# Kernel tuning notes

Hardware: AMD Instinct MI355X
Metric: run time of the kernel (lower is better)

## Reference

```python
import jax, jax.numpy as jnp
import numpy as np

B, DIN, E, FACTOR, STEPS, NH = 2048, 1024, 1024, 16, 3, 8
DH = E // NH
EPS = 1e-5


def layernorm(x, g, b):
    m = x.mean(-1, keepdims=True)
    v = ((x - m) ** 2).mean(-1, keepdims=True)
    return (x - m) / jnp.sqrt(v + EPS) * g + b


def setup_inputs() -> dict:
    key = jax.random.key(0)
    ks = iter(jax.random.split(key, 32))
    r = lambda shape, s=0.02: jax.random.normal(next(ks), shape, dtype=jnp.float32) * s
    F = E * FACTOR
    return {
        "image_feat": jax.random.normal(next(ks), (B, DIN), dtype=jnp.float32),
        "text_feat": jax.random.normal(next(ks), (B, DIN), dtype=jnp.float32),
        # fusion block
        "fc1_w": r((F, DIN)), "fc1_b": jnp.zeros((F,), jnp.float32),
        "fc2_w": r((F, DIN)), "fc2_b": jnp.zeros((F,), jnp.float32),
        "fc3_w": r((E, F)), "fc3_b": jnp.zeros((E,), jnp.float32),
        "ln_g": jnp.ones((E,), jnp.float32), "ln_b": jnp.zeros((E,), jnp.float32),
        # per-step MHA + FFN + norms, stacked over STEPS
        "Wqkv": r((STEPS, 3 * E, E)), "bqkv": jnp.zeros((STEPS, 3 * E), jnp.float32),
        "Wo": r((STEPS, E, E)), "bo": jnp.zeros((STEPS, E), jnp.float32),
        "W1": r((STEPS, E, E)), "b1": jnp.zeros((STEPS, E), jnp.float32),
        "W2": r((STEPS, E, E)), "b2": jnp.zeros((STEPS, E), jnp.float32),
        "n1_g": jnp.ones((STEPS, E), jnp.float32), "n1_b": jnp.zeros((STEPS, E), jnp.float32),
        "n2_g": jnp.ones((STEPS, E), jnp.float32), "n2_b": jnp.zeros((STEPS, E), jnp.float32),
        # output projection
        "Wout": r((DIN, E)), "bout": jnp.zeros((DIN,), jnp.float32),
    }


def mha_step(q, ctx, Wqkv, bqkv, Wo, bo):
    # q: [B,E] (query len 1), ctx: [B,L,E]
    Wq, Wk, Wv = Wqkv[:E], Wqkv[E:2 * E], Wqkv[2 * E:]
    bq, bk, bv = bqkv[:E], bqkv[E:2 * E], bqkv[2 * E:]
    L = ctx.shape[1]
    qh = (q @ Wq.T + bq).reshape(B, NH, DH)
    kh = (ctx @ Wk.T + bk).reshape(B, L, NH, DH)
    vh = (ctx @ Wv.T + bv).reshape(B, L, NH, DH)
    scores = jnp.einsum("bhd,blhd->bhl", qh, kh) / jnp.sqrt(jnp.float32(DH))
    attn = jax.nn.softmax(scores, axis=-1)
    out = jnp.einsum("bhl,blhd->bhd", attn, vh).reshape(B, E)
    return out @ Wo.T + bo


def reference(image_feat, text_feat, fc1_w, fc1_b, fc2_w, fc2_b, fc3_w, fc3_b,
              ln_g, ln_b, Wqkv, bqkv, Wo, bo, W1, b1, W2, b2,
              n1_g, n1_b, n2_g, n2_b, Wout, bout):
    # fusion block (dropout = identity in eval)
    fused = (image_feat @ fc1_w.T + fc1_b) * (text_feat @ fc2_w.T + fc2_b)
    fused = layernorm(fused @ fc3_w.T + fc3_b, ln_g, ln_b)  # [B,E]
    ctx = fused[:, None, :]  # [B,1,E]
    x = fused
    for i in range(STEPS):
        attn = mha_step(x, ctx, Wqkv[i], bqkv[i], Wo[i], bo[i])
        x = x + layernorm(attn, n1_g[i], n1_b[i])
        ffn = jax.nn.relu(x @ W1[i].T + b1[i]) @ W2[i].T + b2[i]
        x = x + layernorm(ffn, n2_g[i], n2_b[i])
        ctx = jnp.concatenate([ctx, x[:, None, :]], axis=1)
    final_output = x @ Wout.T + bout  # [B,DIN]
    return final_output, ctx
```

## Files before the change

### kernel.cpp

```cpp
#include <hip/hip_runtime.h>

#define TB 256

typedef __attribute__((ext_vector_type(8))) short short8;
typedef __attribute__((ext_vector_type(4))) float f32x4;
typedef unsigned short u16;

constexpr int B_  = 2048;
constexpr int DIN = 1024;
constexpr int E   = 1024;
constexpr int F   = 16384;
constexpr int E3  = 3072;
constexpr int CH  = 4096;
constexpr int FH  = 8192;

__device__ __forceinline__ u16 f2bf(float f) {
  union { float f; unsigned u; } v; v.f = f;
  unsigned r = v.u + 0x7fffu + ((v.u >> 16) & 1u);
  return (u16)(r >> 16);
}
__device__ __forceinline__ float bf2f(u16 u) {
  union { unsigned u; float f; } v; v.u = ((unsigned)u) << 16;
  return v.f;
}

__device__ __forceinline__ void gload16(const void* g, void* l) {
  __builtin_amdgcn_global_load_lds(
      (const __attribute__((address_space(1))) void*)g,
      (__attribute__((address_space(3))) void*)l, 16, 0, 0);
}

__device__ __forceinline__ void tile_xy(int& tx, int& ty) {
  int gx = gridDim.x;
  int nwg = gx * gridDim.y;
  int wg = blockIdx.y * gx + blockIdx.x;
  if ((nwg & 7) == 0) wg = (wg & 7) * (nwg >> 3) + (wg >> 3);
  tx = wg % gx; ty = wg / gx;
}

__device__ __forceinline__ int swz16(int o) {
  return o ^ (((o >> 7) & 7) << 4);
}

__global__ __launch_bounds__(256) void cvt_kernel(const float* __restrict__ s,
                                                  u16* __restrict__ d, int n) {
  int i = (blockIdx.x * 256 + threadIdx.x) * 4;
  if (i >= n) return;
  float4 v = *(const float4*)&s[i];
  ushort4 o;
  o.x = f2bf(v.x); o.y = f2bf(v.y); o.z = f2bf(v.z); o.w = f2bf(v.w);
  *(ushort4*)&d[i] = o;
}

__global__ __launch_bounds__(256) void fill_kernel(float* p, int n, float v) {
  int i = blockIdx.x * 256 + threadIdx.x;
  if (i < n) p[i] = v;
}

__global__ __launch_bounds__(256) void relu_bias_cvt_kernel(
    const float* __restrict__ hF, const float* __restrict__ bias,
    u16* __restrict__ out) {
  size_t i = ((size_t)blockIdx.x * 256 + threadIdx.x) * 4;
  int col = (int)(i & 1023);
  float4 v = *(const float4*)&hF[i];
  float4 b = *(const float4*)&bias[col];
  ushort4 o;
  float x0 = v.x + b.x, x1 = v.y + b.y, x2 = v.z + b.z, x3 = v.w + b.w;
  o.x = f2bf(x0 > 0.f ? x0 : 0.f);
  o.y = f2bf(x1 > 0.f ? x1 : 0.f);
  o.z = f2bf(x2 > 0.f ? x2 : 0.f);
  o.w = f2bf(x3 > 0.f ? x3 : 0.f);
  *(ushort4*)&out[i] = o;
}

__global__ __launch_bounds__(256) void bias_add_kernel(
    float* __restrict__ out, const float* __restrict__ bias) {
  size_t i = ((size_t)blockIdx.x * 256 + threadIdx.x) * 4;
  int col = (int)(i & 1023);
  float4 v = *(const float4*)&out[i];
  float4 b = *(const float4*)&bias[col];
  v.x += b.x; v.y += b.y; v.z += b.z; v.w += b.w;
  *(float4*)&out[i] = v;
}

template <int EPI>
__global__ __launch_bounds__(512, 2) void gemm256(
    const u16* __restrict__ A, int sA,
    const u16* __restrict__ Bw, int sB,
    const float* __restrict__ bias, const u16* __restrict__ gate,
    void* __restrict__ Out, int ldOut, int ksz) {
  __shared__ __align__(16) char smem[131072];
  const int tid = threadIdx.x, lane = tid & 63, w = tid >> 6;
  const int wm = w >> 2, wn = w & 3;
  int tx, ty; tile_xy(tx, ty);
  const int m0 = tx * 256, n0 = ty * 256;
  const int k0 = blockIdx.z * ksz;
  const int nt = ksz >> 6;
  const int lr = lane & 15;

  f32x4 acc[8][4] = {};

  auto stage = [&](const u16* __restrict__ G, int gs, int gr0, int kk, int tb, int j) {
    int P = j * 8192 + w * 1024 + lane * 16;
    int L = swz16(P);
    int row = L >> 7, colb = L & 127;
    gload16(G + (size_t)(gr0 + row) * gs + kk + (colb >> 1),
            &smem[tb + j * 8192 + w * 1024]);
  };
  auto rdA = [&](int tb, int mf, int kh) -> short8 {
    int Lo = (wm * 128 + mf * 16 + lr) * 128 + kh * 64 + (lane >> 4) * 16;
    return *(const short8*)&smem[tb + swz16(Lo)];
  };
  auto rdB = [&](int tb, int nf, int kh) -> short8 {
    int Lo = (wn * 64 + nf * 16 + lr) * 128 + kh * 64 + (lane >> 4) * 16;
    return *(const short8*)&smem[tb + swz16(Lo)];
  };

#pragma unroll
  for (int j = 0; j < 4; ++j) stage(A, sA, m0, k0, 0, j);
#pragma unroll
  for (int j = 0; j < 4; ++j) stage(Bw, sB, n0, k0, 65536, j);
  asm volatile("s_waitcnt vmcnt(0)" ::: "memory");
  __builtin_amdgcn_sched_barrier(0);
  __builtin_amdgcn_s_barrier();

  int cur = 0;
  for (int t = 0; t < nt; ++t) {
    const int sa = cur * 32768;
    const int sb = 65536 + cur * 32768;
    if (t + 1 < nt) {
      const int sa2 = (cur ^ 1) * 32768;
      const int sb2 = 65536 + (cur ^ 1) * 32768;
#pragma unroll
      for (int j = 0; j < 4; ++j) stage(A, sA, m0, k0 + (t + 1) * 64, sa2, j);
#pragma unroll
      for (int j = 0; j < 4; ++j) stage(Bw, sB, n0, k0 + (t + 1) * 64, sb2, j);
    }
    short8 bfr[4][2], afr[4][2];
#pragma unroll
    for (int nf = 0; nf < 4; ++nf)
#pragma unroll
      for (int kh = 0; kh < 2; ++kh) bfr[nf][kh] = rdB(sb, nf, kh);
#pragma unroll
    for (int mf = 0; mf < 4; ++mf)
#pragma unroll
      for (int kh = 0; kh < 2; ++kh) afr[mf][kh] = rdA(sa, mf, kh);
    __builtin_amdgcn_s_setprio(1);
#pragma unroll
    for (int mf = 0; mf < 4; ++mf)
#pragma unroll
      for (int nf = 0; nf < 4; ++nf)
#pragma unroll
        for (int kh = 0; kh < 2; ++kh)
          acc[mf][nf] = __builtin_amdgcn_mfma_f32_16x16x32_bf16(
              afr[mf][kh], bfr[nf][kh], acc[mf][nf], 0, 0, 0);
    __builtin_amdgcn_s_setprio(0);
#pragma unroll
    for (int mf = 0; mf < 4; ++mf)
#pragma unroll
      for (int kh = 0; kh < 2; ++kh) afr[mf][kh] = rdA(sa, 4 + mf, kh);
    __builtin_amdgcn_s_setprio(1);
#pragma unroll
    for (int mf = 0; mf < 4; ++mf)
#pragma unroll
      for (int nf = 0; nf < 4; ++nf)
#pragma unroll
        for (int kh = 0; kh < 2; ++kh)
          acc[4 + mf][nf] = __builtin_amdgcn_mfma_f32_16x16x32_bf16(
              afr[mf][kh], bfr[nf][kh], acc[4 + mf][nf], 0, 0, 0);
    __builtin_amdgcn_s_setprio(0);
    if (t + 1 < nt) {
      asm volatile("s_waitcnt vmcnt(0)" ::: "memory");
      __builtin_amdgcn_sched_barrier(0);
      __builtin_amdgcn_s_barrier();
    }
    cur ^= 1;
  }

  const int rb = (lane >> 4) * 4;
#pragma unroll
  for (int mf = 0; mf < 8; ++mf) {
#pragma unroll
    for (int nf = 0; nf < 4; ++nf) {
      int row0 = m0 + wm * 128 + mf * 16 + rb;
      int col  = n0 + wn * 64 + nf * 16 + lr;
      float bv = (EPI == 3 || bias == nullptr) ? 0.f : bias[col];
#pragma unroll
      for (int r = 0; r < 4; ++r) {
        float v = acc[mf][nf][r] + bv;
        size_t idx = (size_t)(row0 + r) * ldOut + col;
        if (EPI == 1)      ((u16*)Out)[idx] = f2bf(v);
        else if (EPI == 3) atomicAdd((float*)Out + idx, v);
        else if (EPI == 4) ((u16*)Out)[idx] = f2bf(v * bf2f(gate[idx]));
        else               ((float*)Out)[idx] = v;
      }
    }
  }
}

template <int EPI>
__global__ __launch_bounds__(TB) void gemm_bt(
    const u16* __restrict__ A, int sA,
    const u16* __restrict__ Bw, int sB,
    const float* __restrict__ bias, const u16* __restrict__ gate,
    void* __restrict__ Out, int ldOut, int Kext, int ksz) {
  __shared__ u16 As[128 * 32];
  __shared__ u16 Bs[128 * 32];
  const int tid = threadIdx.x, lane = tid & 63, w = tid >> 6;
  const int wr = w >> 1, wc = w & 1;
  int tx, ty; tile_xy(tx, ty);
  const int m0 = tx * 128, n0 = ty * 128;
  const int k0 = blockIdx.z * ksz;
  const int kend = min(k0 + ksz, Kext);

  f32x4 acc[4][4] = {};
  const int lr = lane & 15, lk = (lane >> 4) * 8;

  for (int kk = k0; kk < kend; kk += 32) {
#pragma unroll
    for (int is = 0; is < 2; ++is) {
      int c = is * 256 + tid;
      int r = c >> 2, kc = (c & 3) << 3;
      size_t lb = (size_t)(is * 256 + w * 64) * 8;
      gload16(A  + (size_t)(m0 + r) * sA + kk + kc, &As[lb]);
      gload16(Bw + (size_t)(n0 + r) * sB + kk + kc, &Bs[lb]);
    }
    __syncthreads();
    short8 af[4], bfv[4];
#pragma unroll
    for (int m = 0; m < 4; ++m)
      af[m] = *(const short8*)&As[(wr * 64 + m * 16 + lr) * 32 + lk];
#pragma unroll
    for (int n = 0; n < 4; ++n)
      bfv[n] = *(const short8*)&Bs[(wc * 64 + n * 16 + lr) * 32 + lk];
#pragma unroll
    for (int m = 0; m < 4; ++m)
#pragma unroll
      for (int n = 0; n < 4; ++n)
        acc[m][n] = __builtin_amdgcn_mfma_f32_16x16x32_bf16(af[m], bfv[n], acc[m][n], 0, 0, 0);
    __syncthreads();
  }

  const int rbase = (lane >> 4) * 4;
#pragma unroll
  for (int m = 0; m < 4; ++m) {
#pragma unroll
    for (int n = 0; n < 4; ++n) {
      int row0 = m0 + wr * 64 + m * 16 + rbase;
      int col  = n0 + wc * 64 + n * 16 + lr;
      float bv = (EPI == 3 || bias == nullptr) ? 0.f : bias[col];
#pragma unroll
      for (int r = 0; r < 4; ++r) {
        float v = acc[m][n][r] + bv;
        size_t idx = (size_t)(row0 + r) * ldOut + col;
        if (EPI == 0)      ((float*)Out)[idx] = v;
        else if (EPI == 1) ((u16*)Out)[idx] = f2bf(v);
        else if (EPI == 2) ((u16*)Out)[idx] = f2bf(v > 0.f ? v : 0.f);
        else if (EPI == 3) atomicAdd((float*)Out + idx, v);
        else               ((u16*)Out)[idx] = f2bf(v * bf2f(gate[idx]));
      }
    }
  }
}

template <int EPI>
__global__ __launch_bounds__(TB) void gemm_wf32(
    const u16* __restrict__ A, int sA,
    const float* __restrict__ Bw, int sB,
    const float* __restrict__ bias, void* __restrict__ Out, int ldOut,
    int Kext, int ksz) {
  __shared__ u16 As[128 * 32];
  __shared__ u16 Bs[128 * 32];
  const int tid = threadIdx.x, lane = tid & 63, w = tid >> 6;
  const int wr = w >> 1, wc = w & 1;
  int tx, ty; tile_xy(tx, ty);
  const int m0 = tx * 128, n0 = ty * 128;
  const int k0 = blockIdx.z * ksz;
  const int kend = min(k0 + ksz, Kext);

  f32x4 acc[4][4] = {};
  const int lr = lane & 15, lk = (lane >> 4) * 8;

  for (int kk = k0; kk < kend; kk += 32) {
#pragma unroll
    for (int is = 0; is < 2; ++is) {
      int c = is * 256 + tid;
      int r = c >> 2, kc = (c & 3) << 3;
      gload16(A + (size_t)(m0 + r) * sA + kk + kc,
              &As[(size_t)(is * 256 + w * 64) * 8]);
    }
#pragma unroll
    for (int p = 0; p < 4; ++p) {
      int t = tid + p * 256;
      int r = t >> 3, c4 = (t & 7) << 2;
      float4 v = *(const float4*)&Bw[(size_t)(n0 + r) * sB + kk + c4];
      ushort4 o;
      o.x = f2bf(v.x); o.y = f2bf(v.y); o.z = f2bf(v.z); o.w = f2bf(v.w);
      *(ushort4*)&Bs[r * 32 + c4] = o;
    }
    __syncthreads();
    short8 af[4], bfv[4];
#pragma unroll
    for (int m = 0; m < 4; ++m)
      af[m] = *(const short8*)&As[(wr * 64 + m * 16 + lr) * 32 + lk];
#pragma unroll
    for (int n = 0; n < 4; ++n)
      bfv[n] = *(const short8*)&Bs[(wc * 64 + n * 16 + lr) * 32 + lk];
#pragma unroll
    for (int m = 0; m < 4; ++m)
#pragma unroll
      for (int n = 0; n < 4; ++n)
        acc[m][n] = __builtin_amdgcn_mfma_f32_16x16x32_bf16(af[m], bfv[n], acc[m][n], 0, 0, 0);
    __syncthreads();
  }

  const int rbase = (lane >> 4) * 4;
#pragma unroll
  for (int m = 0; m < 4; ++m) {
#pragma unroll
    for (int n = 0; n < 4; ++n) {
      int row0 = m0 + wr * 64 + m * 16 + rbase;
      int col  = n0 + wc * 64 + n * 16 + lr;
      float bv = (EPI == 3 || bias == nullptr) ? 0.f : bias[col];
#pragma unroll
      for (int r = 0; r < 4; ++r) {
        float v = acc[m][n][r] + bv;
        size_t idx = (size_t)(row0 + r) * ldOut + col;
        if (EPI == 0)      ((float*)Out)[idx] = v;
        else if (EPI == 1) ((u16*)Out)[idx] = f2bf(v);
        else if (EPI == 2) ((u16*)Out)[idx] = f2bf(v > 0.f ? v : 0.f);
        else               atomicAdd((float*)Out + idx, v);
      }
    }
  }
}

__global__ __launch_bounds__(TB) void gemm_dual_wf32(
    const u16* __restrict__ A1, const u16* __restrict__ A2, int sA,
    const float* __restrict__ B1, const float* __restrict__ B2, int sB,
    const float* __restrict__ bias1, const float* __restrict__ bias2,
    u16* __restrict__ Out, int ldOut, int K) {
  __shared__ u16 As1[128 * 32];
  __shared__ u16 As2[128 * 32];
  __shared__ u16 Bs1[128 * 32];
  __shared__ u16 Bs2[128 * 32];
  const int tid = threadIdx.x, lane = tid & 63, w = tid >> 6;
  const int wr = w >> 1, wc = w & 1;
  int tx, ty; tile_xy(tx, ty);
  const int m0 = tx * 128, n0 = ty * 128;

  f32x4 acc1[4][4] = {};
  f32x4 acc2[4][4] = {};
  const int lr = lane & 15, lk = (lane >> 4) * 8;

  for (int kk = 0; kk < K; kk += 32) {
#pragma unroll
    for (int is = 0; is < 2; ++is) {
      int c = is * 256 + tid;
      int r = c >> 2, kc = (c & 3) << 3;
      size_t lb = (size_t)(is * 256 + w * 64) * 8;
      gload16(A1 + (size_t)(m0 + r) * sA + kk + kc, &As1[lb]);
      gload16(A2 + (size_t)(m0 + r) * sA + kk + kc, &As2[lb]);
    }
#pragma unroll
    for (int p = 0; p < 4; ++p) {
      int t = tid + p * 256;
      int r = t >> 3, c4 = (t & 7) << 2;
      float4 v1 = *(const float4*)&B1[(size_t)(n0 + r) * sB + kk + c4];
      float4 v2 = *(const float4*)&B2[(size_t)(n0 + r) * sB + kk + c4];
      ushort4 o1, o2;
      o1.x = f2bf(v1.x); o1.y = f2bf(v1.y); o1.z = f2bf(v1.z); o1.w = f2bf(v1.w);
      o2.x = f2bf(v2.x); o2.y = f2bf(v2.y); o2.z = f2bf(v2.z); o2.w = f2bf(v2.w);
      *(ushort4*)&Bs1[r * 32 + c4] = o1;
      *(ushort4*)&Bs2[r * 32 + c4] = o2;
    }
    __syncthreads();
    short8 a1[4], a2[4], b1v[4], b2v[4];
#pragma unroll
    for (int m = 0; m < 4; ++m) {
      a1[m] = *(const short8*)&As1[(wr * 64 + m * 16 + lr) * 32 + lk];
      a2[m] = *(const short8*)&As2[(wr * 64 + m * 16 + lr) * 32 + lk];
    }
#pragma unroll
    for (int n = 0; n < 4; ++n) {
      b1v[n] = *(const short8*)&Bs1[(wc * 64 + n * 16 + lr) * 32 + lk];
      b2v[n] = *(const short8*)&Bs2[(wc * 64 + n * 16 + lr) * 32 + lk];
    }
#pragma unroll
    for (int m = 0; m < 4; ++m)
#pragma unroll
      for (int n = 0; n < 4; ++n) {
        acc1[m][n] = __builtin_amdgcn_mfma_f32_16x16x32_bf16(a1[m], b1v[n], acc1[m][n], 0, 0, 0);
        acc2[m][n] = __builtin_amdgcn_mfma_f32_16x16x32_bf16(a2[m], b2v[n], acc2[m][n], 0, 0, 0);
      }
    __syncthreads();
  }

  const int rbase = (lane >> 4) * 4;
#pragma unroll
  for (int m = 0; m < 4; ++m) {
#pragma unroll
    for (int n = 0; n < 4; ++n) {
      int row0 = m0 + wr * 64 + m * 16 + rbase;
      int col  = n0 + wc * 64 + n * 16 + lr;
      float bv1 = bias1[col], bv2 = bias2[col];
#pragma unroll
      for (int r = 0; r < 4; ++r) {
        float v = (acc1[m][n][r] + bv1) * (acc2[m][n][r] + bv2);
        Out[(size_t)(row0 + r) * ldOut + col] = f2bf(v);
      }
    }
  }
}

template <int MODE>
__global__ __launch_bounds__(256) void resln_kernel(
    const float* __restrict__ Y, const float* __restrict__ preb,
    const float* __restrict__ g, const float* __restrict__ bp,
    float* __restrict__ x, u16* __restrict__ xb,
    float* __restrict__ ctxo, int ctxRow) {
  const int r = blockIdx.x, tid = threadIdx.x;
  const size_t base = (size_t)r * 1024 + tid * 4;
  float4 y4 = *(const float4*)&Y[base];
  float y[4] = {y4.x, y4.y, y4.z, y4.w};
  if (preb != nullptr) {
    float4 p4 = *(const float4*)&preb[tid * 4];
    y[0] += p4.x; y[1] += p4.y; y[2] += p4.z; y[3] += p4.w;
  }
  float s = y[0] + y[1] + y[2] + y[3];
  float q = y[0] * y[0] + y[1] * y[1] + y[2] * y[2] + y[3] * y[3];
  __shared__ float red[8];
  for (int o = 32; o; o >>= 1) { s += __shfl_xor(s, o); q += __shfl_xor(q, o); }
  int wv = tid >> 6;
  if ((tid & 63) == 0) { red[wv] = s; red[4 + wv] = q; }
  __syncthreads();
  s = red[0] + red[1] + red[2] + red[3];
  q = red[4] + red[5] + red[6] + red[7];
  float mean = s * (1.f / 1024.f);
  float var  = q * (1.f / 1024.f) - mean * mean;
  float rs   = rsqrtf(var + 1e-5f);
  float4 g4 = *(const float4*)&g[tid * 4];
  float4 b4 = *(const float4*)&bp[tid * 4];
  float gg[4] = {g4.x, g4.y, g4.z, g4.w};
  float bb[4] = {b4.x, b4.y, b4.z, b4.w};
  float xv[4];
#pragma unroll
  for (int j = 0; j < 4; ++j) {
    float val = (y[j] - mean) * rs * gg[j] + bb[j];
    xv[j] = (MODE == 0) ? val : x[base + j] + val;
  }
  *(float4*)&x[base] = make_float4(xv[0], xv[1], xv[2], xv[3]);
  ushort4 xo;
  xo.x = f2bf(xv[0]); xo.y = f2bf(xv[1]); xo.z = f2bf(xv[2]); xo.w = f2bf(xv[3]);
  *(ushort4*)&xb[base] = xo;
  if (MODE != 1) {
    size_t cb = ((size_t)r * 4 + ctxRow) * 1024 + tid * 4;
    *(float4*)&ctxo[cb] = make_float4(xv[0], xv[1], xv[2], xv[3]);
  }
}

__global__ __launch_bounds__(64) void attn_kernel(const u16* __restrict__ qkv,
                                                  u16* __restrict__ out, int L) {
  const int b = blockIdx.x >> 3, h = blockIdx.x & 7;
  const int lane = threadIdx.x;
  const size_t qoff = ((size_t)(L - 1) * B_ + b) * E3 + h * 128;
  float q0 = bf2f(qkv[qoff + lane]);
  float q1 = bf2f(qkv[qoff + 64 + lane]);
  float sc[3];
  for (int l = 0; l < L; ++l) {
    size_t kb = ((size_t)l * B_ + b) * E3 + 1024 + h * 128;
    float p = q0 * bf2f(qkv[kb + lane]) + q1 * bf2f(qkv[kb + 64 + lane]);
    for (int o = 32; o; o >>= 1) p += __shfl_xor(p, o);
    sc[l] = p * 0.08838834764831843f;
  }
  float m = sc[0];
  for (int l = 1; l < L; ++l) m = fmaxf(m, sc[l]);
  float wsum = 0.f, wgt[3];
  for (int l = 0; l < L; ++l) { wgt[l] = expf(sc[l] - m); wsum += wgt[l]; }
  float inv = 1.f / wsum;
  float o0 = 0.f, o1 = 0.f;
  for (int l = 0; l < L; ++l) {
    size_t vb = ((size_t)l * B_ + b) * E3 + 2048 + h * 128;
    o0 += wgt[l] * bf2f(qkv[vb + lane]);
    o1 += wgt[l] * bf2f(qkv[vb + 64 + lane]);
  }
  out[(size_t)b * 1024 + h * 128 + lane]      = f2bf(o0 * inv);
  out[(size_t)b * 1024 + h * 128 + 64 + lane] = f2bf(o1 * inv);
}

extern "C" void kernel_launch(void* const* d_in, const int* in_sizes, int n_in,
                              void* d_out, int out_size, void* d_ws, size_t ws_size,
                              hipStream_t stream) {
  (void)in_sizes; (void)n_in;
  const float* image = (const float*)d_in[0];
  const float* text  = (const float*)d_in[1];
  const float* fc1_w = (const float*)d_in[2];
  const float* fc1_b = (const float*)d_in[3];
  const float* fc2_w = (const float*)d_in[4];
  const float* fc2_b = (const float*)d_in[5];
  const float* fc3_w = (const float*)d_in[6];
  const float* fc3_b = (const float*)d_in[7];
  const float* ln_g  = (const float*)d_in[8];
  const float* ln_b  = (const float*)d_in[9];
  const float* Wqkv  = (const float*)d_in[10];
  const float* bqkv  = (const float*)d_in[11];
  const float* Wo    = (const float*)d_in[12];
  const float* bo    = (const float*)d_in[13];
  const float* W1    = (const float*)d_in[14];
  const float* b1    = (const float*)d_in[15];
  const float* W2    = (const float*)d_in[16];
  const float* b2    = (const float*)d_in[17];
  const float* n1_g  = (const float*)d_in[18];
  const float* n1_b  = (const float*)d_in[19];
  const float* n2_g  = (const float*)d_in[20];
  const float* n2_b  = (const float*)d_in[21];
  const float* WoutW = (const float*)d_in[22];
  const float* boutW = (const float*)d_in[23];

  float* outF   = (float*)d_out;
  float* ctxOut = outF + (size_t)B_ * DIN;
  char* ws = (char*)d_ws;

  auto cvt = [&](const float* s, u16* d, size_t n) {
    cvt_kernel<<<dim3((unsigned)((n + 1023) / 1024)), 256, 0, stream>>>(s, d, (int)n);
  };

  const size_t NEED_A = 232783872;
  if (ws_size >= NEED_A) {
    size_t off = 0;
    auto carve = [&](size_t bytes) -> char* {
      char* p = ws + off; off += (bytes + 255) & ~(size_t)255; return p;
    };
    u16* imgB  = (u16*)carve((size_t)B_ * DIN * 2);
    u16* txtB  = (u16*)carve((size_t)B_ * DIN * 2);
    u16* fc1B  = (u16*)carve((size_t)F * DIN * 2);
    u16* fc2B  = (u16*)carve((size_t)F * DIN * 2);
    u16* fc3B  = (u16*)carve((size_t)E * F * 2);
    u16* WqkvB = (u16*)carve((size_t)3 * E3 * E * 2);
    u16* WoB   = (u16*)carve((size_t)3 * E * E * 2);
    u16* W1B   = (u16*)carve((size_t)3 * E * E * 2);
    u16* W2B   = (u16*)carve((size_t)3 * E * E * 2);
    u16* WoutB = (u16*)carve((size_t)DIN * E * 2);
    char* U    = carve((size_t)B_ * F * 2);
    float* xF  = (float*)carve((size_t)B_ * E * 4);
    float* hF  = (float*)carve((size_t)B_ * E * 4);
    u16* g1B    = (u16*)U;
    u16* fusedC = (u16*)(U + (size_t)B_ * FH * 2);
    u16* qkvB   = (u16*)(U);
    u16* ctxB   = (u16*)(U + 37748736);
    u16* attnB  = (u16*)(U + 37748736 + 16777216);
    u16* h1B    = (u16*)(U + 37748736 + 16777216 + 4194304);
    u16* xbB    = (u16*)(U + 37748736 + 16777216 + 8388608);

    cvt(image, imgB, (size_t)B_ * DIN);
    cvt(text,  txtB, (size_t)B_ * DIN);
    cvt(fc1_w, fc1B, (size_t)F * DIN);
    cvt(fc2_w, fc2B, (size_t)F * DIN);
    cvt(fc3_w, fc3B, (size_t)E * F);
    cvt(Wqkv,  WqkvB, (size_t)3 * E3 * E);
    cvt(Wo,    WoB,   (size_t)3 * E * E);
    cvt(W1,    W1B,   (size_t)3 * E * E);
    cvt(W2,    W2B,   (size_t)3 * E * E);
    cvt(WoutW, WoutB, (size_t)DIN * E);
    hipMemsetAsync(hF, 0, (size_t)B_ * E * 4, stream);

    for (int c = 0; c < 2; ++c) {
      gemm256<1><<<dim3(B_ / 256, FH / 256), 512, 0, stream>>>(
          imgB, DIN, fc1B + (size_t)c * FH * DIN, DIN,
          fc1_b + (size_t)c * FH, nullptr, g1B, FH, DIN);
      gemm256<4><<<dim3(B_ / 256, FH / 256), 512, 0, stream>>>(
          txtB, DIN, fc2B + (size_t)c * FH * DIN, DIN,
          fc2_b + (size_t)c * FH, g1B, fusedC, FH, DIN);
      gemm256<3><<<dim3(B_ / 256, E / 256, 8), 512, 0, stream>>>(
          fusedC, FH, fc3B + (size_t)c * FH, F, nullptr, nullptr, hF, E, FH / 8);
    }

    resln_kernel<0><<<B_, 256, 0, stream>>>(hF, fc3_b, ln_g, ln_b, xF, ctxB, ctxOut, 0);

    for (int i = 0; i < 3; ++i) {
      int L = i + 1;
      gemm256<1><<<dim3(L * B_ / 256, E3 / 256), 512, 0, stream>>>(
          ctxB, E, WqkvB + (size_t)i * E3 * E, E, bqkv + (size_t)i * E3, nullptr,
          qkvB, E3, E);
      attn_kernel<<<B_ * 8, 64, 0, stream>>>(qkvB, attnB, L);
      hipMemsetAsync(hF, 0, (size_t)B_ * E * 4, stream);
      gemm_bt<3><<<dim3(B_ / 128, E / 128, 2), TB, 0, stream>>>(
          attnB, E, WoB + (size_t)i * E * E, E, nullptr, nullptr, hF, E, E, E / 2);
      resln_kernel<1><<<B_, 256, 0, stream>>>(
          hF, bo + (size_t)i * E, n1_g + (size_t)i * E, n1_b + (size_t)i * E,
          xF, xbB, nullptr, 0);
      hipMemsetAsync(hF, 0, (size_t)B_ * E * 4, stream);
      gemm_bt<3><<<dim3(B_ / 128, E / 128, 2), TB, 0, stream>>>(
          xbB, E, W1B + (size_t)i * E * E, E, nullptr, nullptr, hF, E, E, E / 2);
      relu_bias_cvt_kernel<<<B_ * E / 1024, 256, 0, stream>>>(
          hF, b1 + (size_t)i * E, h1B);
      hipMemsetAsync(hF, 0, (size_t)B_ * E * 4, stream);
      gemm_bt<3><<<dim3(B_ / 128, E / 128, 2), TB, 0, stream>>>(
          h1B, E, W2B + (size_t)i * E * E, E, nullptr, nullptr, hF, E, E, E / 2);
      resln_kernel<2><<<B_, 256, 0, stream>>>(
          hF, b2 + (size_t)i * E, n2_g + (size_t)i * E, n2_b + (size_t)i * E,
          xF, ctxB + (size_t)(i + 1) * B_ * E, ctxOut, i + 1);
    }

    hipMemsetAsync(outF, 0, (size_t)B_ * DIN * 4, stream);
    gemm_bt<3><<<dim3(B_ / 128, DIN / 128, 2), TB, 0, stream>>>(
        ctxB + (size_t)3 * B_ * E, E, WoutB, E, nullptr, nullptr, outF, DIN, E, E / 2);
    bias_add_kernel<<<B_ * DIN / 1024, 256, 0, stream>>>(outF, boutW);
    return;
  }

  size_t off = 0;
  auto carve = [&](size_t bytes) -> char* {
    char* p = ws + off; off += (bytes + 255) & ~(size_t)255; return p;
  };
  u16* imgB   = (u16*)carve((size_t)B_ * DIN * 2);
  u16* txtB   = (u16*)carve((size_t)B_ * DIN * 2);
  u16* fusedC = (u16*)carve((size_t)B_ * CH * 2);
  u16* qkvB   = (u16*)carve((size_t)3 * B_ * E3 * 2);
  u16* ctxB   = (u16*)carve((size_t)4 * B_ * E * 2);
  u16* attnB  = (u16*)carve((size_t)B_ * E * 2);
  u16* h1B    = (u16*)carve((size_t)B_ * E * 2);
  u16* xbB    = (u16*)carve((size_t)B_ * E * 2);
  float* xF   = (float*)carve((size_t)B_ * E * 4);
  float* hF   = (float*)carve((size_t)B_ * E * 4);

  if (off > ws_size) {
    fill_kernel<<<(out_size + 255) / 256, 256, 0, stream>>>(outF, out_size, 12345.0f);
    return;
  }

  cvt(image, imgB, (size_t)B_ * DIN);
  cvt(text,  txtB, (size_t)B_ * DIN);
  hipMemsetAsync(hF, 0, (size_t)B_ * E * 4, stream);

  for (int c = 0; c < F / CH; ++c) {
    gemm_dual_wf32<<<dim3(B_ / 128, CH / 128), TB, 0, stream>>>(
        imgB, txtB, DIN,
        fc1_w + (size_t)c * CH * DIN, fc2_w + (size_t)c * CH * DIN, DIN,
        fc1_b + (size_t)c * CH, fc2_b + (size_t)c * CH, fusedC, CH, DIN);
    gemm_wf32<3><<<dim3(B_ / 128, E / 128, 2), TB, 0, stream>>>(
        fusedC, CH, fc3_w + (size_t)c * CH, F, nullptr, hF, E, CH, CH / 2);
  }
  resln_kernel<0><<<B_, 256, 0, stream>>>(hF, fc3_b, ln_g, ln_b, xF, ctxB, ctxOut, 0);

  for (int i = 0; i < 3; ++i) {
    int L = i + 1;
    gemm_wf32<1><<<dim3(L * B_ / 128, E3 / 128), TB, 0, stream>>>(
        ctxB, E, Wqkv + (size_t)i * E3 * E, E, bqkv + (size_t)i * E3, qkvB, E3, E, E);
    attn_kernel<<<B_ * 8, 64, 0, stream>>>(qkvB, attnB, L);
    gemm_wf32<0><<<dim3(B_ / 128, E / 128), TB, 0, stream>>>(
        attnB, E, Wo + (size_t)i * E * E, E, bo + (size_t)i * E, hF, E, E, E);
    resln_kernel<1><<<B_, 256, 0, stream>>>(
        hF, nullptr, n1_g + (size_t)i * E, n1_b + (size_t)i * E, xF, xbB, nullptr, 0);
    gemm_wf32<2><<<dim3(B_ / 128, E / 128), TB, 0, stream>>>(
        xbB, E, W1 + (size_t)i * E * E, E, b1 + (size_t)i * E, h1B, E, E, E);
    gemm_wf32<0><<<dim3(B_ / 128, E / 128), TB, 0, stream>>>(
        h1B, E, W2 + (size_t)i * E * E, E, b2 + (size_t)i * E, hF, E, E, E);
    resln_kernel<2><<<B_, 256, 0, stream>>>(
        hF, nullptr, n2_g + (size_t)i * E, n2_b + (size_t)i * E, xF,
        ctxB + (size_t)(i + 1) * B_ * E, ctxOut, i + 1);
  }
  gemm_wf32<0><<<dim3(B_ / 128, DIN / 128), TB, 0, stream>>>(
      ctxB + (size_t)3 * B_ * E, E, WoutW, E, boutW, outF, DIN, E, E);
}
```

Measured before the change: 950.3 us.

## Replace atomic split-K with two partial buffers and fuse partial sums downstream

```diff
diff --git a/kernel.cpp b/kernel.cpp
--- a/kernel.cpp
+++ b/kernel.cpp
@@ -12,7 +12,6 @@
 constexpr int F   = 16384;
 constexpr int E3  = 3072;
 constexpr int CH  = 4096;
-constexpr int FH  = 8192;
 
 __device__ __forceinline__ u16 f2bf(float f) {
   union { float f; unsigned u; } v; v.f = f;
@@ -57,15 +56,17 @@
   if (i < n) p[i] = v;
 }
 
-__global__ __launch_bounds__(256) void relu_bias_cvt_kernel(
-    const float* __restrict__ hF, const float* __restrict__ bias,
-    u16* __restrict__ out) {
+__global__ __launch_bounds__(256) void relu_bias2_kernel(
+    const float* __restrict__ Y0, const float* __restrict__ Y1,
+    const float* __restrict__ bias, u16* __restrict__ out) {
   size_t i = ((size_t)blockIdx.x * 256 + threadIdx.x) * 4;
   int col = (int)(i & 1023);
-  float4 v = *(const float4*)&hF[i];
+  float4 a = *(const float4*)&Y0[i];
+  float4 c = *(const float4*)&Y1[i];
   float4 b = *(const float4*)&bias[col];
+  float x0 = a.x + c.x + b.x, x1 = a.y + c.y + b.y;
+  float x2 = a.z + c.z + b.z, x3 = a.w + c.w + b.w;
   ushort4 o;
-  float x0 = v.x + b.x, x1 = v.y + b.y, x2 = v.z + b.z, x3 = v.w + b.w;
   o.x = f2bf(x0 > 0.f ? x0 : 0.f);
   o.y = f2bf(x1 > 0.f ? x1 : 0.f);
   o.z = f2bf(x2 > 0.f ? x2 : 0.f);
@@ -73,14 +74,18 @@
   *(ushort4*)&out[i] = o;
 }
 
-__global__ __launch_bounds__(256) void bias_add_kernel(
-    float* __restrict__ out, const float* __restrict__ bias) {
+__global__ __launch_bounds__(256) void combine_out_kernel(
+    const float* __restrict__ P0, const float* __restrict__ P1,
+    const float* __restrict__ bias, float* __restrict__ out) {
   size_t i = ((size_t)blockIdx.x * 256 + threadIdx.x) * 4;
   int col = (int)(i & 1023);
-  float4 v = *(const float4*)&out[i];
+  float4 a = *(const float4*)&P0[i];
+  float4 c = *(const float4*)&P1[i];
   float4 b = *(const float4*)&bias[col];
-  v.x += b.x; v.y += b.y; v.z += b.z; v.w += b.w;
-  *(float4*)&out[i] = v;
+  out[i]     = a.x + c.x + b.x;
+  out[i + 1] = a.y + c.y + b.y;
+  out[i + 2] = a.z + c.z + b.z;
+  out[i + 3] = a.w + c.w + b.w;
 }
 
 template <int EPI>
@@ -94,7 +99,6 @@
   const int wm = w >> 2, wn = w & 3;
   int tx, ty; tile_xy(tx, ty);
   const int m0 = tx * 256, n0 = ty * 256;
-  const int k0 = blockIdx.z * ksz;
   const int nt = ksz >> 6;
   const int lr = lane & 15;
 
@@ -117,9 +121,9 @@
   };
 
 #pragma unroll
-  for (int j = 0; j < 4; ++j) stage(A, sA, m0, k0, 0, j);
-#pragma unroll
-  for (int j = 0; j < 4; ++j) stage(Bw, sB, n0, k0, 65536, j);
+  for (int j = 0; j < 4; ++j) stage(A, sA, m0, 0, 0, j);
+#pragma unroll
+  for (int j = 0; j < 4; ++j) stage(Bw, sB, n0, 0, 65536, j);
   asm volatile("s_waitcnt vmcnt(0)" ::: "memory");
   __builtin_amdgcn_sched_barrier(0);
   __builtin_amdgcn_s_barrier();
@@ -132,9 +136,9 @@
       const int sa2 = (cur ^ 1) * 32768;
       const int sb2 = 65536 + (cur ^ 1) * 32768;
 #pragma unroll
-      for (int j = 0; j < 4; ++j) stage(A, sA, m0, k0 + (t + 1) * 64, sa2, j);
-#pragma unroll
-      for (int j = 0; j < 4; ++j) stage(Bw, sB, n0, k0 + (t + 1) * 64, sb2, j);
+      for (int j = 0; j < 4; ++j) stage(A, sA, m0, (t + 1) * 64, sa2, j);
+#pragma unroll
+      for (int j = 0; j < 4; ++j) stage(Bw, sB, n0, (t + 1) * 64, sb2, j);
     }
     short8 bfr[4][2], afr[4][2];
 #pragma unroll
@@ -184,15 +188,13 @@
     for (int nf = 0; nf < 4; ++nf) {
       int row0 = m0 + wm * 128 + mf * 16 + rb;
       int col  = n0 + wn * 64 + nf * 16 + lr;
-      float bv = (EPI == 3 || bias == nullptr) ? 0.f : bias[col];
+      float bv = (bias == nullptr) ? 0.f : bias[col];
 #pragma unroll
       for (int r = 0; r < 4; ++r) {
         float v = acc[mf][nf][r] + bv;
         size_t idx = (size_t)(row0 + r) * ldOut + col;
-        if (EPI == 1)      ((u16*)Out)[idx] = f2bf(v);
-        else if (EPI == 3) atomicAdd((float*)Out + idx, v);
-        else if (EPI == 4) ((u16*)Out)[idx] = f2bf(v * bf2f(gate[idx]));
-        else               ((float*)Out)[idx] = v;
+        if (EPI == 4) ((u16*)Out)[idx] = f2bf(v * bf2f(gate[idx]));
+        else          ((u16*)Out)[idx] = f2bf(v);
       }
     }
   }
@@ -202,8 +204,9 @@
 __global__ __launch_bounds__(TB) void gemm_bt(
     const u16* __restrict__ A, int sA,
     const u16* __restrict__ Bw, int sB,
-    const float* __restrict__ bias, const u16* __restrict__ gate,
-    void* __restrict__ Out, int ldOut, int Kext, int ksz) {
+    const float* __restrict__ bias,
+    void* __restrict__ Out, void* __restrict__ Out2,
+    int ldOut, int Kext, int ksz) {
   __shared__ u16 As[128 * 32];
   __shared__ u16 Bs[128 * 32];
   const int tid = threadIdx.x, lane = tid & 63, w = tid >> 6;
@@ -241,6 +244,8 @@
     __syncthreads();
   }
 
+  float* Of = (EPI == 0 && Out2 != nullptr && blockIdx.z != 0) ? (float*)Out2
+                                                               : (float*)Out;
   const int rbase = (lane >> 4) * 4;
 #pragma unroll
   for (int m = 0; m < 4; ++m) {
@@ -248,16 +253,13 @@
     for (int n = 0; n < 4; ++n) {
       int row0 = m0 + wr * 64 + m * 16 + rbase;
       int col  = n0 + wc * 64 + n * 16 + lr;
-      float bv = (EPI == 3 || bias == nullptr) ? 0.f : bias[col];
+      float bv = (bias == nullptr) ? 0.f : bias[col];
 #pragma unroll
       for (int r = 0; r < 4; ++r) {
         float v = acc[m][n][r] + bv;
         size_t idx = (size_t)(row0 + r) * ldOut + col;
-        if (EPI == 0)      ((float*)Out)[idx] = v;
-        else if (EPI == 1) ((u16*)Out)[idx] = f2bf(v);
-        else if (EPI == 2) ((u16*)Out)[idx] = f2bf(v > 0.f ? v : 0.f);
-        else if (EPI == 3) atomicAdd((float*)Out + idx, v);
-        else               ((u16*)Out)[idx] = f2bf(v * bf2f(gate[idx]));
+        if (EPI == 0) Of[idx] = v;
+        else          ((u16*)Out)[idx] = f2bf(v);
       }
     }
   }
@@ -415,14 +417,19 @@
 
 template <int MODE>
 __global__ __launch_bounds__(256) void resln_kernel(
-    const float* __restrict__ Y, const float* __restrict__ preb,
+    const float* __restrict__ Y0, const float* __restrict__ Y1,
+    const float* __restrict__ preb,
     const float* __restrict__ g, const float* __restrict__ bp,
     float* __restrict__ x, u16* __restrict__ xb,
     float* __restrict__ ctxo, int ctxRow) {
   const int r = blockIdx.x, tid = threadIdx.x;
   const size_t base = (size_t)r * 1024 + tid * 4;
-  float4 y4 = *(const float4*)&Y[base];
+  float4 y4 = *(const float4*)&Y0[base];
   float y[4] = {y4.x, y4.y, y4.z, y4.w};
+  if (Y1 != nullptr) {
+    float4 z4 = *(const float4*)&Y1[base];
+    y[0] += z4.x; y[1] += z4.y; y[2] += z4.z; y[3] += z4.w;
+  }
   if (preb != nullptr) {
     float4 p4 = *(const float4*)&preb[tid * 4];
     y[0] += p4.x; y[1] += p4.y; y[2] += p4.z; y[3] += p4.w;
@@ -544,13 +551,13 @@
     char* U    = carve((size_t)B_ * F * 2);
     float* xF  = (float*)carve((size_t)B_ * E * 4);
     float* hF  = (float*)carve((size_t)B_ * E * 4);
-    u16* g1B    = (u16*)U;
-    u16* fusedC = (u16*)(U + (size_t)B_ * FH * 2);
+    u16* fusedB = (u16*)U;
     u16* qkvB   = (u16*)(U);
     u16* ctxB   = (u16*)(U + 37748736);
     u16* attnB  = (u16*)(U + 37748736 + 16777216);
     u16* h1B    = (u16*)(U + 37748736 + 16777216 + 4194304);
     u16* xbB    = (u16*)(U + 37748736 + 16777216 + 8388608);
+    float* finP1 = (float*)qkvB;
 
     cvt(image, imgB, (size_t)B_ * DIN);
     cvt(text,  txtB, (size_t)B_ * DIN);
@@ -562,50 +569,41 @@
     cvt(W1,    W1B,   (size_t)3 * E * E);
     cvt(W2,    W2B,   (size_t)3 * E * E);
     cvt(WoutW, WoutB, (size_t)DIN * E);
-    hipMemsetAsync(hF, 0, (size_t)B_ * E * 4, stream);
-
-    for (int c = 0; c < 2; ++c) {
-      gemm256<1><<<dim3(B_ / 256, FH / 256), 512, 0, stream>>>(
-          imgB, DIN, fc1B + (size_t)c * FH * DIN, DIN,
-          fc1_b + (size_t)c * FH, nullptr, g1B, FH, DIN);
-      gemm256<4><<<dim3(B_ / 256, FH / 256), 512, 0, stream>>>(
-          txtB, DIN, fc2B + (size_t)c * FH * DIN, DIN,
-          fc2_b + (size_t)c * FH, g1B, fusedC, FH, DIN);
-      gemm256<3><<<dim3(B_ / 256, E / 256, 8), 512, 0, stream>>>(
-          fusedC, FH, fc3B + (size_t)c * FH, F, nullptr, nullptr, hF, E, FH / 8);
-    }
-
-    resln_kernel<0><<<B_, 256, 0, stream>>>(hF, fc3_b, ln_g, ln_b, xF, ctxB, ctxOut, 0);
+
+    gemm256<1><<<dim3(B_ / 256, F / 256), 512, 0, stream>>>(
+        txtB, DIN, fc2B, DIN, fc2_b, nullptr, fusedB, F, DIN);
+    gemm256<4><<<dim3(B_ / 256, F / 256), 512, 0, stream>>>(
+        imgB, DIN, fc1B, DIN, fc1_b, fusedB, fusedB, F, DIN);
+    gemm_bt<0><<<dim3(B_ / 128, E / 128, 2), TB, 0, stream>>>(
+        fusedB, F, fc3B, F, nullptr, xF, hF, E, F, F / 2);
+    resln_kernel<0><<<B_, 256, 0, stream>>>(
+        xF, hF, fc3_b, ln_g, ln_b, xF, ctxB, ctxOut, 0);
 
     for (int i = 0; i < 3; ++i) {
       int L = i + 1;
-      gemm256<1><<<dim3(L * B_ / 256, E3 / 256), 512, 0, stream>>>(
-          ctxB, E, WqkvB + (size_t)i * E3 * E, E, bqkv + (size_t)i * E3, nullptr,
-          qkvB, E3, E);
+      gemm_bt<1><<<dim3(L * B_ / 128, E3 / 128), TB, 0, stream>>>(
+          ctxB, E, WqkvB + (size_t)i * E3 * E, E, bqkv + (size_t)i * E3,
+          qkvB, nullptr, E3, E, E);
       attn_kernel<<<B_ * 8, 64, 0, stream>>>(qkvB, attnB, L);
-      hipMemsetAsync(hF, 0, (size_t)B_ * E * 4, stream);
-      gemm_bt<3><<<dim3(B_ / 128, E / 128, 2), TB, 0, stream>>>(
-          attnB, E, WoB + (size_t)i * E * E, E, nullptr, nullptr, hF, E, E, E / 2);
+      gemm_bt<0><<<dim3(B_ / 128, E / 128, 2), TB, 0, stream>>>(
+          attnB, E, WoB + (size_t)i * E * E, E, nullptr, hF, outF, E, E, E / 2);
       resln_kernel<1><<<B_, 256, 0, stream>>>(
-          hF, bo + (size_t)i * E, n1_g + (size_t)i * E, n1_b + (size_t)i * E,
+          hF, outF, bo + (size_t)i * E, n1_g + (size_t)i * E, n1_b + (size_t)i * E,
           xF, xbB, nullptr, 0);
-      hipMemsetAsync(hF, 0, (size_t)B_ * E * 4, stream);
-      gemm_bt<3><<<dim3(B_ / 128, E / 128, 2), TB, 0, stream>>>(
-          xbB, E, W1B + (size_t)i * E * E, E, nullptr, nullptr, hF, E, E, E / 2);
-      relu_bias_cvt_kernel<<<B_ * E / 1024, 256, 0, stream>>>(
-          hF, b1 + (size_t)i * E, h1B);
-      hipMemsetAsync(hF, 0, (size_t)B_ * E * 4, stream);
-      gemm_bt<3><<<dim3(B_ / 128, E / 128, 2), TB, 0, stream>>>(
-          h1B, E, W2B + (size_t)i * E * E, E, nullptr, nullptr, hF, E, E, E / 2);
+      gemm_bt<0><<<dim3(B_ / 128, E / 128, 2), TB, 0, stream>>>(
+          xbB, E, W1B + (size_t)i * E * E, E, nullptr, hF, outF, E, E, E / 2);
+      relu_bias2_kernel<<<B_ * E / 1024, 256, 0, stream>>>(
+          hF, outF, b1 + (size_t)i * E, h1B);
+      gemm_bt<0><<<dim3(B_ / 128, E / 128, 2), TB, 0, stream>>>(
+          h1B, E, W2B + (size_t)i * E * E, E, nullptr, hF, outF, E, E, E / 2);
       resln_kernel<2><<<B_, 256, 0, stream>>>(
-          hF, b2 + (size_t)i * E, n2_g + (size_t)i * E, n2_b + (size_t)i * E,
+          hF, outF, b2 + (size_t)i * E, n2_g + (size_t)i * E, n2_b + (size_t)i * E,
           xF, ctxB + (size_t)(i + 1) * B_ * E, ctxOut, i + 1);
     }
 
-    hipMemsetAsync(outF, 0, (size_t)B_ * DIN * 4, stream);
-    gemm_bt<3><<<dim3(B_ / 128, DIN / 128, 2), TB, 0, stream>>>(
-        ctxB + (size_t)3 * B_ * E, E, WoutB, E, nullptr, nullptr, outF, DIN, E, E / 2);
-    bias_add_kernel<<<B_ * DIN / 1024, 256, 0, stream>>>(outF, boutW);
+    gemm_bt<0><<<dim3(B_ / 128, DIN / 128, 2), TB, 0, stream>>>(
+        ctxB + (size_t)3 * B_ * E, E, WoutB, E, nullptr, hF, finP1, DIN, E, E / 2);
+    combine_out_kernel<<<B_ * DIN / 1024, 256, 0, stream>>>(hF, finP1, boutW, outF);
     return;
   }
 
@@ -641,7 +639,7 @@
     gemm_wf32<3><<<dim3(B_ / 128, E / 128, 2), TB, 0, stream>>>(
         fusedC, CH, fc3_w + (size_t)c * CH, F, nullptr, hF, E, CH, CH / 2);
   }
-  resln_kernel<0><<<B_, 256, 0, stream>>>(hF, fc3_b, ln_g, ln_b, xF, ctxB, ctxOut, 0);
+  resln_kernel<0><<<B_, 256, 0, stream>>>(hF, nullptr, fc3_b, ln_g, ln_b, xF, ctxB, ctxOut, 0);
 
   for (int i = 0; i < 3; ++i) {
     int L = i + 1;
@@ -651,13 +649,13 @@
     gemm_wf32<0><<<dim3(B_ / 128, E / 128), TB, 0, stream>>>(
         attnB, E, Wo + (size_t)i * E * E, E, bo + (size_t)i * E, hF, E, E, E);
     resln_kernel<1><<<B_, 256, 0, stream>>>(
-        hF, nullptr, n1_g + (size_t)i * E, n1_b + (size_t)i * E, xF, xbB, nullptr, 0);
+        hF, nullptr, nullptr, n1_g + (size_t)i * E, n1_b + (size_t)i * E, xF, xbB, nullptr, 0);
     gemm_wf32<2><<<dim3(B_ / 128, E / 128), TB, 0, stream>>>(
         xbB, E, W1 + (size_t)i * E * E, E, b1 + (size_t)i * E, h1B, E, E, E);
     gemm_wf32<0><<<dim3(B_ / 128, E / 128), TB, 0, stream>>>(
         h1B, E, W2 + (size_t)i * E * E, E, b2 + (size_t)i * E, hF, E, E, E);
     resln_kernel<2><<<B_, 256, 0, stream>>>(
-        hF, nullptr, n2_g + (size_t)i * E, n2_b + (size_t)i * E, xF,
+        hF, nullptr, nullptr, n2_g + (size_t)i * E, n2_b + (size_t)i * E, xF,
         ctxB + (size_t)(i + 1) * B_ * E, ctxOut, i + 1);
   }
   gemm_wf32<0><<<dim3(B_ / 128, DIN / 128), TB, 0, stream>>>(
```

Result: slower. 977.9 us (+2.9%).
